# Optimization experiments

Measured on AMD Instinct MI355X. Metric: run time of the kernel, lower is better.

The kernel has to match this reference:

```python
import math
import jax, jax.numpy as jnp
import numpy as np

H = 12
D_MODEL = 768
D_K = D_MODEL // H
B, S = 2, 2048


def setup_inputs() -> dict:
    key = jax.random.key(0)
    ks = jax.random.split(key, 12)
    sc = 0.02
    inp = {
        "query": jax.random.normal(ks[0], (B, S, D_MODEL), jnp.float32),
        "key": jax.random.normal(ks[1], (B, S, D_MODEL), jnp.float32),
        "value": jax.random.normal(ks[2], (B, S, D_MODEL), jnp.float32),
        # causal mask [B, S, S]: 1 where attendable
        "mask": jnp.broadcast_to(jnp.tril(jnp.ones((S, S), jnp.int32)), (B, S, S)),
        "Wq": sc * jax.random.normal(ks[3], (D_MODEL, D_MODEL), jnp.float32),
        "bq": jnp.zeros((D_MODEL,), jnp.float32),
        "Wk": sc * jax.random.normal(ks[4], (D_MODEL, D_MODEL), jnp.float32),
        "bk": jnp.zeros((D_MODEL,), jnp.float32),
        "Wv": sc * jax.random.normal(ks[5], (D_MODEL, D_MODEL), jnp.float32),
        "bv": jnp.zeros((D_MODEL,), jnp.float32),
        "Wo": sc * jax.random.normal(ks[6], (D_MODEL, D_MODEL), jnp.float32),
        "bo": jnp.zeros((D_MODEL,), jnp.float32),
    }
    return inp


def reference(query, key, value, mask, Wq, bq, Wk, bk, Wv, bv, Wo, bo):
    b, s, _ = query.shape
    # linear projections (torch Linear: x @ W.T + b), split into heads
    def proj(x, W, bias):
        return (x @ W.T + bias).reshape(b, s, H, D_K).transpose(0, 2, 1, 3)  # [B,H,S,Dk]

    q = proj(query, Wq, bq)
    k = proj(key, Wk, bk)
    v = proj(value, Wv, bv)

    scores = jnp.einsum("bhqd,bhkd->bhqk", q, k) / math.sqrt(D_K)  # [B,H,S,S]
    # exponential time-decay bias over key positions 1..S, shape [1,1,1,S]
    time = jnp.exp(-jnp.arange(1, s + 1, dtype=scores.dtype))[None, None, None, :]
    scores = jnp.where(mask[:, None, :, :] == 0, jnp.asarray(-1e9, scores.dtype), scores)
    p_attn = jax.nn.softmax(scores - time, axis=-1)
    x = jnp.einsum("bhqk,bhkd->bhqd", p_attn, v)  # [B,H,S,Dk]
    x = x.transpose(0, 2, 1, 3).reshape(b, s, H * D_K)
    return x @ Wo.T + bo
```

## Files before the change

kernel.cpp:

```cpp
#include <hip/hip_runtime.h>
#include <hip/hip_bf16.h>
#include <math.h>

typedef __bf16 bf16;
typedef __attribute__((ext_vector_type(8))) __bf16 bf16x8;
typedef __attribute__((ext_vector_type(4))) __bf16 bf16x4;
typedef __attribute__((ext_vector_type(4))) float floatx4;

#define NH 12
#define DK 64
#define DM 768
#define NB 2
#define SEQ 2048
#define MTOT (NB * SEQ)
#define WELEM (DM * DM)
#define XELEM (MTOT * DM)

static __device__ __forceinline__ bf16x8 load8(const bf16* p) {
    return *(const bf16x8*)p;
}
static __device__ __forceinline__ float4 ld4(const float* p) {
    return *(const float4*)p;
}
static __device__ __forceinline__ bf16x8 cvt8(const float4 a, const float4 b) {
    bf16x8 r;
    r[0] = (bf16)a.x; r[1] = (bf16)a.y; r[2] = (bf16)a.z; r[3] = (bf16)a.w;
    r[4] = (bf16)b.x; r[5] = (bf16)b.y; r[6] = (bf16)b.z; r[7] = (bf16)b.w;
    return r;
}
static __device__ __forceinline__ void async16(const bf16* g, bf16* l) {
    __builtin_amdgcn_global_load_lds((const __attribute__((address_space(1))) void*)g,
                                     (__attribute__((address_space(3))) void*)l,
                                     16, 0, 0);
}

__global__ __launch_bounds__(256) void cvt_kernel(
    const float* __restrict__ wq, const float* __restrict__ wk,
    const float* __restrict__ wv, const float* __restrict__ wo,
    const float* __restrict__ xq, const float* __restrict__ xk, const float* __restrict__ xv,
    bf16* __restrict__ Wb, bf16* __restrict__ Wob,
    bf16* __restrict__ Xqb, bf16* __restrict__ Xkb, bf16* __restrict__ Xvb) {
    const int g = blockIdx.x * 256 + threadIdx.x;
    const int PW = WELEM / 8;
    const int PX = XELEM / 8;
    if (g < 4 * PW) {
        const int wi = g / PW;
        const int rem = g - wi * PW;
        const int n = rem / 96;
        const int t = rem - n * 96;
        const int s = t >> 3;
        const int j = t & 7;
        const float* src = (wi == 0) ? wq : (wi == 1) ? wk : (wi == 2) ? wv : wo;
        bf16* dst = (wi < 3) ? (Wb + (size_t)wi * WELEM) : Wob;
        const float* p = src + (size_t)n * DM + s * 64 + j * 8;
        *(bf16x8*)(dst + (size_t)n * DM + s * 64 + ((j ^ (n & 7)) * 8)) = cvt8(ld4(p), ld4(p + 4));
    } else {
        const int gx = g - 4 * PW;
        const int xi = gx / PX;
        const int rem = gx - xi * PX;
        const int m = rem / 96;
        const int t = rem - m * 96;
        const int s = t >> 3;
        const int j = t & 7;
        const float* src = (xi == 0) ? xq : (xi == 1) ? xk : xv;
        bf16* dst = (xi == 0) ? Xqb : (xi == 1) ? Xkb : Xvb;
        const float* p = src + (size_t)m * DM + s * 64 + j * 8;
        *(bf16x8*)(dst + (size_t)m * DM + s * 64 + ((j ^ (m & 7)) * 8)) = cvt8(ld4(p), ld4(p + 4));
    }
}

__global__ __launch_bounds__(256, 3) void qkv_kernel(
    const bf16* __restrict__ Xqb, const bf16* __restrict__ Xkb, const bf16* __restrict__ Xvb,
    const bf16* __restrict__ Wb,
    const float* __restrict__ bq, const float* __restrict__ bk, const float* __restrict__ bv,
    bf16* __restrict__ Oq, bf16* __restrict__ Ok, bf16* __restrict__ Ov) {
    __shared__ __align__(16) bf16 SM[2 * 64 * 64 + 2 * 128 * 64];
    bf16* As0 = SM;
    bf16* Bs0 = SM + 8192;

    const int tid = threadIdx.x;
    const int id = blockIdx.x;
    const int xcd = id & 7;
    const int sl = id >> 3;
    const int z = sl / 48;
    const int r = sl % 48;
    const int m0 = (xcd * 8 + r / 6) * 64;
    const int n0 = (r % 6) * 128;

    const bf16* X = (z == 0) ? Xqb : (z == 1) ? Xkb : Xvb;
    const bf16* W = Wb + (size_t)z * WELEM;
    const float* bias = (z == 0) ? bq : (z == 1) ? bk : bv;
    bf16* out = (z == 0) ? Oq : (z == 1) ? Ok : Ov;

    const int wv = tid >> 6;
    const int wm = wv >> 1, wn = wv & 1;
    const int lane = tid & 63;
    const int ln = lane & 15;
    const int kq = lane >> 4;
    const int drow = lane >> 3;
    const int dcol = (lane & 7) * 8;

    floatx4 acc[2][4];
#pragma unroll
    for (int i = 0; i < 2; i++)
#pragma unroll
        for (int j = 0; j < 4; j++) acc[i][j] = (floatx4){0.f, 0.f, 0.f, 0.f};

#pragma unroll
    for (int it = 0; it < 2; it++)
        async16(X + (size_t)(m0 + wv * 16 + it * 8 + drow) * DM + dcol,
                As0 + (wv * 16 + it * 8) * 64);
#pragma unroll
    for (int it = 0; it < 4; it++)
        async16(W + (size_t)(n0 + wv * 32 + it * 8 + drow) * DM + dcol,
                Bs0 + (wv * 32 + it * 8) * 64);

    for (int k = 0; k < 12; k++) {
        __syncthreads();
        const bf16* Ap = As0 + (k & 1) * 4096;
        const bf16* Bp = Bs0 + (k & 1) * 8192;
        if (k < 11) {
            const int kc = (k + 1) * 64;
            bf16* An = As0 + ((k + 1) & 1) * 4096;
            bf16* Bn = Bs0 + ((k + 1) & 1) * 8192;
#pragma unroll
            for (int it = 0; it < 2; it++)
                async16(X + (size_t)(m0 + wv * 16 + it * 8 + drow) * DM + kc + dcol,
                        An + (wv * 16 + it * 8) * 64);
#pragma unroll
            for (int it = 0; it < 4; it++)
                async16(W + (size_t)(n0 + wv * 32 + it * 8 + drow) * DM + kc + dcol,
                        Bn + (wv * 32 + it * 8) * 64);
        }
#pragma unroll
        for (int ks = 0; ks < 2; ks++) {
            const int jb = (ks * 4 + kq) ^ (ln & 7);
            bf16x8 af[2], bfm[4];
#pragma unroll
            for (int mt = 0; mt < 2; mt++)
                af[mt] = *(const bf16x8*)&Ap[(wm * 32 + mt * 16 + ln) * 64 + jb * 8];
#pragma unroll
            for (int nt = 0; nt < 4; nt++)
                bfm[nt] = *(const bf16x8*)&Bp[(wn * 64 + nt * 16 + ln) * 64 + jb * 8];
#pragma unroll
            for (int mt = 0; mt < 2; mt++)
#pragma unroll
                for (int nt = 0; nt < 4; nt++)
                    acc[mt][nt] = __builtin_amdgcn_mfma_f32_16x16x32_bf16(af[mt], bfm[nt], acc[mt][nt], 0, 0, 0);
        }
    }

    float bv4[4];
#pragma unroll
    for (int nt = 0; nt < 4; nt++) bv4[nt] = bias[n0 + wn * 64 + nt * 16 + ln];

    if (z < 2) {
        __syncthreads();
        bf16 (*E)[136] = (bf16(*)[136])SM;
#pragma unroll
        for (int mt = 0; mt < 2; mt++)
#pragma unroll
            for (int nt = 0; nt < 4; nt++)
#pragma unroll
                for (int r2 = 0; r2 < 4; r2++)
                    E[wm * 32 + mt * 16 + kq * 4 + r2][wn * 64 + nt * 16 + ln] =
                        (bf16)(acc[mt][nt][r2] + bv4[nt]);
        __syncthreads();
        const int row = tid >> 2;
        const int cb = (tid & 3) * 32;
        const int m = m0 + row;
        const int b = m >> 11;
        const int s = m & (SEQ - 1);
        const int h = (n0 + cb) >> 6;
        const int d = (n0 + cb) & 63;
        bf16* op = &out[((size_t)(b * NH + h) * SEQ + s) * DK + d];
#pragma unroll
        for (int q2 = 0; q2 < 4; q2++)
            *(bf16x8*)(op + q2 * 8) = *(bf16x8*)&E[row][cb + q2 * 8];
    } else {
        __syncthreads();
        bf16 (*E)[72] = (bf16(*)[72])SM;
#pragma unroll
        for (int nt = 0; nt < 4; nt++)
#pragma unroll
            for (int mt = 0; mt < 2; mt++) {
                bf16x4 v;
#pragma unroll
                for (int r2 = 0; r2 < 4; r2++) v[r2] = (bf16)(acc[mt][nt][r2] + bv4[nt]);
                *(bf16x4*)&E[wn * 64 + nt * 16 + ln][wm * 32 + mt * 16 + kq * 4] = v;
            }
        __syncthreads();
        const int row = tid >> 1;
        const int sc = (tid & 1) * 32;
        const int b = m0 >> 11;
        const int s0 = m0 & (SEQ - 1);
        const int h = (n0 >> 6) + (row >> 6);
        const int d = row & 63;
        bf16* op = &out[(size_t)(b * NH + h) * DK * SEQ + (size_t)d * SEQ + s0 + sc];
#pragma unroll
        for (int q2 = 0; q2 < 4; q2++)
            *(bf16x8*)(op + q2 * 8) = *(bf16x8*)&E[row][sc + q2 * 8];
    }
}

__global__ __launch_bounds__(256) void attn_kernel(const bf16* __restrict__ Q,
                                                   const bf16* __restrict__ K,
                                                   const bf16* __restrict__ Vt,
                                                   bf16* __restrict__ Xout) {
    __shared__ bf16 Ks[128][72];
    __shared__ bf16 Vs[64][136];
    __shared__ bf16 Ps[4][16][136];

    const int tid = threadIdx.x;
    const int wv = tid >> 6;
    const int lane = tid & 63;
    const int ln = lane & 15;
    const int kq = lane >> 4;
    const int krow = tid >> 1;
    const int kcol = (tid & 1) * 32;
    const int vrow = tid >> 2;
    const int vcol = (tid & 3) * 32;

    const int bidx = blockIdx.x;
    const int rk = (bidx < 256 || bidx >= 512) ? bidx : 767 - bidx;
    const int x = 31 - (rk / 24);
    const int bh = rk % 24;

    const int q0 = x * 64;
    const int qbase = q0 + wv * 16;
    const int nch = (x >> 1) + 1;

    const bf16* Qb = Q + (size_t)bh * SEQ * DK;
    const bf16* Kb = K + (size_t)bh * SEQ * DK;
    const bf16* Vb = Vt + (size_t)bh * SEQ * DK;

    const bf16x8 qa0 = load8(&Qb[(size_t)(qbase + ln) * DK + kq * 8]);
    const bf16x8 qa1 = load8(&Qb[(size_t)(qbase + ln) * DK + 32 + kq * 8]);

    bf16x8 kx[4], vx[4];
#pragma unroll
    for (int q = 0; q < 4; q++) {
        kx[q] = load8(&Kb[(size_t)krow * DK + kcol + q * 8]);
        vx[q] = load8(&Vb[(size_t)vrow * SEQ + vcol + q * 8]);
    }

    float lsum[4] = {0.f, 0.f, 0.f, 0.f};
    floatx4 Oacc[4];
#pragma unroll
    for (int nt = 0; nt < 4; nt++) Oacc[nt] = (floatx4){0.f, 0.f, 0.f, 0.f};

    int qg[4];
#pragma unroll
    for (int r = 0; r < 4; r++) qg[r] = qbase + kq * 4 + r;

    for (int c = 0; c < nch; c++) {
        const int k0 = c * 128;
        __syncthreads();
#pragma unroll
        for (int q = 0; q < 4; q++) {
            *(bf16x8*)&Ks[krow][kcol + q * 8] = kx[q];
            *(bf16x8*)&Vs[vrow][vcol + q * 8] = vx[q];
        }
        __syncthreads();
        if (c + 1 < nch) {
            const int kn = k0 + 128;
#pragma unroll
            for (int q = 0; q < 4; q++) {
                kx[q] = load8(&Kb[(size_t)(kn + krow) * DK + kcol + q * 8]);
                vx[q] = load8(&Vb[(size_t)vrow * SEQ + kn + vcol + q * 8]);
            }
        }

        floatx4 sc[8];
#pragma unroll
        for (int ks = 0; ks < 8; ks++) {
            const bf16x8 b0 = *(bf16x8*)&Ks[ks * 16 + ln][kq * 8];
            const bf16x8 b1 = *(bf16x8*)&Ks[ks * 16 + ln][32 + kq * 8];
            floatx4 t = (floatx4){0.f, 0.f, 0.f, 0.f};
            t = __builtin_amdgcn_mfma_f32_16x16x32_bf16(qa0, b0, t, 0, 0, 0);
            t = __builtin_amdgcn_mfma_f32_16x16x32_bf16(qa1, b1, t, 0, 0, 0);
            sc[ks] = t;
        }

        const bool last = (c == nch - 1);
#pragma unroll
        for (int ks = 0; ks < 8; ks++) {
            const int kg = k0 + ks * 16 + ln;
            const float tb = __expf(-(float)(kg + 1));
#pragma unroll
            for (int r = 0; r < 4; r++) {
                const float sv = sc[ks][r] * 0.125f - tb;
                float pf = __expf(sv);
                if (last && kg > qg[r]) pf = 0.f;
                const bf16 pb = (bf16)pf;
                Ps[wv][kq * 4 + r][ks * 16 + ln] = pb;
                lsum[r] += (float)pb;
            }
        }

        bf16x8 pa[4];
#pragma unroll
        for (int seg = 0; seg < 4; seg++) pa[seg] = *(bf16x8*)&Ps[wv][ln][seg * 32 + kq * 8];
#pragma unroll
        for (int nt = 0; nt < 4; nt++) {
#pragma unroll
            for (int seg = 0; seg < 4; seg++) {
                const bf16x8 vb = *(bf16x8*)&Vs[nt * 16 + ln][seg * 32 + kq * 8];
                Oacc[nt] = __builtin_amdgcn_mfma_f32_16x16x32_bf16(pa[seg], vb, Oacc[nt], 0, 0, 0);
            }
        }
    }

#pragma unroll
    for (int off = 1; off < 16; off <<= 1) {
#pragma unroll
        for (int r = 0; r < 4; r++) lsum[r] += __shfl_xor(lsum[r], off, 64);
    }
    float rl[4];
#pragma unroll
    for (int r = 0; r < 4; r++) rl[r] = 1.f / lsum[r];

    __syncthreads();
    bf16 (*E)[72] = (bf16(*)[72])Ks;
    const int erow = tid >> 2;
    const int ecb = (tid & 3) * 16;
#pragma unroll
    for (int nt = 0; nt < 4; nt++) {
#pragma unroll
        for (int r = 0; r < 4; r++)
            E[wv * 16 + kq * 4 + r][nt * 16 + ln] = (bf16)(Oacc[nt][r] * rl[r]);
    }
    __syncthreads();
    const int b = bh / NH;
    const int h = bh - b * NH;
    const int q = q0 + erow;
    const int j0 = (tid & 3) * 2;
    const int key = erow & 7;
    bf16* rowp = &Xout[((size_t)(b * SEQ + q)) * DM + h * DK];
    *(bf16x8*)(rowp + ((j0 ^ key) * 8)) = *(bf16x8*)&E[erow][ecb];
    *(bf16x8*)(rowp + (((j0 + 1) ^ key) * 8)) = *(bf16x8*)&E[erow][ecb + 8];
}

__global__ __launch_bounds__(256, 3) void outproj_kernel(const bf16* __restrict__ X,
                                                         const bf16* __restrict__ W,
                                                         const float* __restrict__ bias,
                                                         float* __restrict__ out) {
    __shared__ __align__(16) bf16 SM[2 * 64 * 64 + 2 * 128 * 64];
    bf16* As0 = SM;
    bf16* Bs0 = SM + 8192;

    const int tid = threadIdx.x;
    const int id = blockIdx.x;
    const int xcd = id & 7;
    const int sl = id >> 3;
    const int m0 = (xcd * 8 + sl / 6) * 64;
    const int n0 = (sl % 6) * 128;

    const int wv = tid >> 6;
    const int wm = wv >> 1, wn = wv & 1;
    const int lane = tid & 63;
    const int ln = lane & 15;
    const int kq = lane >> 4;
    const int drow = lane >> 3;
    const int dcol = (lane & 7) * 8;

    floatx4 acc[2][4];
#pragma unroll
    for (int i = 0; i < 2; i++)
#pragma unroll
        for (int j = 0; j < 4; j++) acc[i][j] = (floatx4){0.f, 0.f, 0.f, 0.f};

#pragma unroll
    for (int it = 0; it < 2; it++)
        async16(X + (size_t)(m0 + wv * 16 + it * 8 + drow) * DM + dcol,
                As0 + (wv * 16 + it * 8) * 64);
#pragma unroll
    for (int it = 0; it < 4; it++)
        async16(W + (size_t)(n0 + wv * 32 + it * 8 + drow) * DM + dcol,
                Bs0 + (wv * 32 + it * 8) * 64);

    for (int k = 0; k < 12; k++) {
        __syncthreads();
        const bf16* Ap = As0 + (k & 1) * 4096;
        const bf16* Bp = Bs0 + (k & 1) * 8192;
        if (k < 11) {
            const int kc = (k + 1) * 64;
            bf16* An = As0 + ((k + 1) & 1) * 4096;
            bf16* Bn = Bs0 + ((k + 1) & 1) * 8192;
#pragma unroll
            for (int it = 0; it < 2; it++)
                async16(X + (size_t)(m0 + wv * 16 + it * 8 + drow) * DM + kc + dcol,
                        An + (wv * 16 + it * 8) * 64);
#pragma unroll
            for (int it = 0; it < 4; it++)
                async16(W + (size_t)(n0 + wv * 32 + it * 8 + drow) * DM + kc + dcol,
                        Bn + (wv * 32 + it * 8) * 64);
        }
#pragma unroll
        for (int ks = 0; ks < 2; ks++) {
            const int jb = (ks * 4 + kq) ^ (ln & 7);
            bf16x8 af[2], bfm[4];
#pragma unroll
            for (int mt = 0; mt < 2; mt++)
                af[mt] = *(const bf16x8*)&Ap[(wm * 32 + mt * 16 + ln) * 64 + jb * 8];
#pragma unroll
            for (int nt = 0; nt < 4; nt++)
                bfm[nt] = *(const bf16x8*)&Bp[(wn * 64 + nt * 16 + ln) * 64 + jb * 8];
#pragma unroll
            for (int mt = 0; mt < 2; mt++)
#pragma unroll
                for (int nt = 0; nt < 4; nt++)
                    acc[mt][nt] = __builtin_amdgcn_mfma_f32_16x16x32_bf16(af[mt], bfm[nt], acc[mt][nt], 0, 0, 0);
        }
    }

#pragma unroll
    for (int nt = 0; nt < 4; nt++) {
        const int n = n0 + wn * 64 + nt * 16 + ln;
        const float bval = bias[n];
#pragma unroll
        for (int mt = 0; mt < 2; mt++)
#pragma unroll
            for (int r2 = 0; r2 < 4; r2++) {
                const int m = m0 + wm * 32 + mt * 16 + kq * 4 + r2;
                out[(size_t)m * DM + n] = acc[mt][nt][r2] + bval;
            }
    }
}

extern "C" void kernel_launch(void* const* d_in, const int* in_sizes, int n_in,
                              void* d_out, int out_size, void* d_ws, size_t ws_size,
                              hipStream_t stream) {
    const float* query = (const float*)d_in[0];
    const float* key   = (const float*)d_in[1];
    const float* value = (const float*)d_in[2];
    const float* Wq = (const float*)d_in[4];
    const float* bq = (const float*)d_in[5];
    const float* Wk = (const float*)d_in[6];
    const float* bk = (const float*)d_in[7];
    const float* Wv = (const float*)d_in[8];
    const float* bv = (const float*)d_in[9];
    const float* Wo = (const float*)d_in[10];
    const float* bo = (const float*)d_in[11];
    float* out = (float*)d_out;

    bf16* Qws  = (bf16*)d_ws;
    bf16* Kws  = Qws + XELEM;
    bf16* Vtws = Kws + XELEM;
    bf16* Xws  = Vtws + XELEM;
    bf16* Wob  = Xws + XELEM;
    bf16* Xvb  = Wob + WELEM;

    bf16* Wb  = (bf16*)out;
    bf16* Xkb = (bf16*)out + 3 * WELEM;

    bf16* Xqb = Xws;

    const int ncvt = (4 * (WELEM / 8) + 3 * (XELEM / 8)) / 256;
    cvt_kernel<<<ncvt, 256, 0, stream>>>(Wq, Wk, Wv, Wo, query, key, value,
                                         Wb, Wob, Xqb, Xkb, Xvb);

    qkv_kernel<<<1152, 256, 0, stream>>>(Xqb, Xkb, Xvb, Wb, bq, bk, bv,
                                         Qws, Kws, Vtws);

    attn_kernel<<<768, 256, 0, stream>>>(Qws, Kws, Vtws, Xws);

    outproj_kernel<<<384, 256, 0, stream>>>(Xws, Wob, bo, out);
}
```

Before: 195.0 us.

## Double-buffer K/V tiles via async LDS loads with swizzled layout

The attention kernel now streams K and V in 64-key chunks into double-buffered LDS using global_load_lds async copies instead of staging through registers. The projection epilogue pre-swizzles K and Vt rows with an XOR pattern so LDS reads are bank-conflict free without padding. Q is pre-scaled by log2(e)/sqrt(dk) so softmax uses exp2f directly, and the time-decay bias is only computed on the first chunk because it is negligible later. Smaller chunks mean finer causal skipping but twice as many loop iterations and barriers. The bias truncation relies on exp(-k) underflowing in float.

After: 204.1 us. +4.7%, slower.

```diff
diff --git a/kernel.cpp b/kernel.cpp
--- a/kernel.cpp
+++ b/kernel.cpp
@@ -15,6 +15,7 @@
 #define MTOT (NB * SEQ)
 #define WELEM (DM * DM)
 #define XELEM (MTOT * DM)
+#define QSCALE 0.18033688f
 
 static __device__ __forceinline__ bf16x8 load8(const bf16* p) {
     return *(const bf16x8*)p;
@@ -153,6 +154,7 @@
     float bv4[4];
 #pragma unroll
     for (int nt = 0; nt < 4; nt++) bv4[nt] = bias[n0 + wn * 64 + nt * 16 + ln];
+    const float sc = (z == 0) ? QSCALE : 1.0f;
 
     if (z < 2) {
         __syncthreads();
@@ -164,7 +166,7 @@
 #pragma unroll
                 for (int r2 = 0; r2 < 4; r2++)
                     E[wm * 32 + mt * 16 + kq * 4 + r2][wn * 64 + nt * 16 + ln] =
-                        (bf16)(acc[mt][nt][r2] + bv4[nt]);
+                        (bf16)((acc[mt][nt][r2] + bv4[nt]) * sc);
         __syncthreads();
         const int row = tid >> 2;
         const int cb = (tid & 3) * 32;
@@ -172,11 +174,12 @@
         const int b = m >> 11;
         const int s = m & (SEQ - 1);
         const int h = (n0 + cb) >> 6;
-        const int d = (n0 + cb) & 63;
-        bf16* op = &out[((size_t)(b * NH + h) * SEQ + s) * DK + d];
+        const int key = (z == 1) ? (row & 7) : 0;
+        bf16* op = &out[((size_t)(b * NH + h) * SEQ + s) * DK];
+        const int jbase = (cb & 63) >> 3;
 #pragma unroll
         for (int q2 = 0; q2 < 4; q2++)
-            *(bf16x8*)(op + q2 * 8) = *(bf16x8*)&E[row][cb + q2 * 8];
+            *(bf16x8*)(op + ((jbase + q2) ^ key) * 8) = *(bf16x8*)&E[row][cb + q2 * 8];
     } else {
         __syncthreads();
         bf16 (*E)[72] = (bf16(*)[72])SM;
@@ -191,15 +194,17 @@
             }
         __syncthreads();
         const int row = tid >> 1;
-        const int sc = (tid & 1) * 32;
+        const int scc = (tid & 1) * 32;
         const int b = m0 >> 11;
         const int s0 = m0 & (SEQ - 1);
         const int h = (n0 >> 6) + (row >> 6);
         const int d = row & 63;
-        bf16* op = &out[(size_t)(b * NH + h) * DK * SEQ + (size_t)d * SEQ + s0 + sc];
+        const int key = d & 7;
+        bf16* op = &out[(size_t)(b * NH + h) * DK * SEQ + (size_t)d * SEQ + s0];
+        const int jbase = scc >> 3;
 #pragma unroll
         for (int q2 = 0; q2 < 4; q2++)
-            *(bf16x8*)(op + q2 * 8) = *(bf16x8*)&E[row][sc + q2 * 8];
+            *(bf16x8*)(op + ((jbase + q2) ^ key) * 8) = *(bf16x8*)&E[row][scc + q2 * 8];
     }
 }
 
@@ -207,19 +212,17 @@
                                                    const bf16* __restrict__ K,
                                                    const bf16* __restrict__ Vt,
                                                    bf16* __restrict__ Xout) {
-    __shared__ bf16 Ks[128][72];
-    __shared__ bf16 Vs[64][136];
-    __shared__ bf16 Ps[4][16][136];
+    __shared__ __align__(16) bf16 Ks[2][64 * 64];
+    __shared__ __align__(16) bf16 Vs[2][64 * 64];
+    __shared__ bf16 Ps[4][16][68];
 
     const int tid = threadIdx.x;
     const int wv = tid >> 6;
     const int lane = tid & 63;
     const int ln = lane & 15;
     const int kq = lane >> 4;
-    const int krow = tid >> 1;
-    const int kcol = (tid & 1) * 32;
-    const int vrow = tid >> 2;
-    const int vcol = (tid & 3) * 32;
+    const int drow = lane >> 3;
+    const int dcol = (lane & 7) * 8;
 
     const int bidx = blockIdx.x;
     const int rk = (bidx < 256 || bidx >= 512) ? bidx : 767 - bidx;
@@ -228,21 +231,25 @@
 
     const int q0 = x * 64;
     const int qbase = q0 + wv * 16;
-    const int nch = (x >> 1) + 1;
+    const int nch = x + 1;
 
     const bf16* Qb = Q + (size_t)bh * SEQ * DK;
     const bf16* Kb = K + (size_t)bh * SEQ * DK;
     const bf16* Vb = Vt + (size_t)bh * SEQ * DK;
 
+#pragma unroll
+    for (int it = 0; it < 2; it++) {
+        async16(Kb + (size_t)(wv * 16 + it * 8 + drow) * DK + dcol,
+                &Ks[0][(wv * 16 + it * 8) * 64]);
+        async16(Vb + (size_t)(wv * 16 + it * 8 + drow) * SEQ + dcol,
+                &Vs[0][(wv * 16 + it * 8) * 64]);
+    }
+
     const bf16x8 qa0 = load8(&Qb[(size_t)(qbase + ln) * DK + kq * 8]);
     const bf16x8 qa1 = load8(&Qb[(size_t)(qbase + ln) * DK + 32 + kq * 8]);
 
-    bf16x8 kx[4], vx[4];
-#pragma unroll
-    for (int q = 0; q < 4; q++) {
-        kx[q] = load8(&Kb[(size_t)krow * DK + kcol + q * 8]);
-        vx[q] = load8(&Vb[(size_t)vrow * SEQ + vcol + q * 8]);
-    }
+    const int e0 = (kq ^ (ln & 7)) * 8;
+    const int e1 = ((kq + 4) ^ (ln & 7)) * 8;
 
     float lsum[4] = {0.f, 0.f, 0.f, 0.f};
     floatx4 Oacc[4];
@@ -254,60 +261,55 @@
     for (int r = 0; r < 4; r++) qg[r] = qbase + kq * 4 + r;
 
     for (int c = 0; c < nch; c++) {
-        const int k0 = c * 128;
-        __syncthreads();
-#pragma unroll
-        for (int q = 0; q < 4; q++) {
-            *(bf16x8*)&Ks[krow][kcol + q * 8] = kx[q];
-            *(bf16x8*)&Vs[vrow][vcol + q * 8] = vx[q];
-        }
+        const int k0 = c * 64;
+        const int buf = c & 1;
         __syncthreads();
         if (c + 1 < nch) {
-            const int kn = k0 + 128;
-#pragma unroll
-            for (int q = 0; q < 4; q++) {
-                kx[q] = load8(&Kb[(size_t)(kn + krow) * DK + kcol + q * 8]);
-                vx[q] = load8(&Vb[(size_t)vrow * SEQ + kn + vcol + q * 8]);
+            const int kn = k0 + 64;
+            const int nb = buf ^ 1;
+#pragma unroll
+            for (int it = 0; it < 2; it++) {
+                async16(Kb + (size_t)(kn + wv * 16 + it * 8 + drow) * DK + dcol,
+                        &Ks[nb][(wv * 16 + it * 8) * 64]);
+                async16(Vb + (size_t)(wv * 16 + it * 8 + drow) * SEQ + kn + dcol,
+                        &Vs[nb][(wv * 16 + it * 8) * 64]);
             }
         }
 
-        floatx4 sc[8];
-#pragma unroll
-        for (int ks = 0; ks < 8; ks++) {
-            const bf16x8 b0 = *(bf16x8*)&Ks[ks * 16 + ln][kq * 8];
-            const bf16x8 b1 = *(bf16x8*)&Ks[ks * 16 + ln][32 + kq * 8];
+        floatx4 sc[4];
+#pragma unroll
+        for (int ks = 0; ks < 4; ks++) {
+            const bf16x8 b0 = *(const bf16x8*)&Ks[buf][(ks * 16 + ln) * 64 + e0];
+            const bf16x8 b1 = *(const bf16x8*)&Ks[buf][(ks * 16 + ln) * 64 + e1];
             floatx4 t = (floatx4){0.f, 0.f, 0.f, 0.f};
             t = __builtin_amdgcn_mfma_f32_16x16x32_bf16(qa0, b0, t, 0, 0, 0);
             t = __builtin_amdgcn_mfma_f32_16x16x32_bf16(qa1, b1, t, 0, 0, 0);
             sc[ks] = t;
         }
 
-        const bool last = (c == nch - 1);
-#pragma unroll
-        for (int ks = 0; ks < 8; ks++) {
+        const bool last = (c == x);
+#pragma unroll
+        for (int ks = 0; ks < 4; ks++) {
             const int kg = k0 + ks * 16 + ln;
-            const float tb = __expf(-(float)(kg + 1));
+            float tb2 = 0.f;
+            if (c == 0) tb2 = 1.44269504f * __expf(-(float)(kg + 1));
 #pragma unroll
             for (int r = 0; r < 4; r++) {
-                const float sv = sc[ks][r] * 0.125f - tb;
-                float pf = __expf(sv);
+                float pf = exp2f(sc[ks][r] - tb2);
                 if (last && kg > qg[r]) pf = 0.f;
-                const bf16 pb = (bf16)pf;
-                Ps[wv][kq * 4 + r][ks * 16 + ln] = pb;
-                lsum[r] += (float)pb;
+                Ps[wv][kq * 4 + r][ks * 16 + ln] = (bf16)pf;
+                lsum[r] += pf;
             }
         }
 
-        bf16x8 pa[4];
-#pragma unroll
-        for (int seg = 0; seg < 4; seg++) pa[seg] = *(bf16x8*)&Ps[wv][ln][seg * 32 + kq * 8];
+        const bf16x8 pa0 = *(const bf16x8*)&Ps[wv][ln][kq * 8];
+        const bf16x8 pa1 = *(const bf16x8*)&Ps[wv][ln][32 + kq * 8];
 #pragma unroll
         for (int nt = 0; nt < 4; nt++) {
-#pragma unroll
-            for (int seg = 0; seg < 4; seg++) {
-                const bf16x8 vb = *(bf16x8*)&Vs[nt * 16 + ln][seg * 32 + kq * 8];
-                Oacc[nt] = __builtin_amdgcn_mfma_f32_16x16x32_bf16(pa[seg], vb, Oacc[nt], 0, 0, 0);
-            }
+            const bf16x8 v0 = *(const bf16x8*)&Vs[buf][(nt * 16 + ln) * 64 + e0];
+            const bf16x8 v1 = *(const bf16x8*)&Vs[buf][(nt * 16 + ln) * 64 + e1];
+            Oacc[nt] = __builtin_amdgcn_mfma_f32_16x16x32_bf16(pa0, v0, Oacc[nt], 0, 0, 0);
+            Oacc[nt] = __builtin_amdgcn_mfma_f32_16x16x32_bf16(pa1, v1, Oacc[nt], 0, 0, 0);
         }
     }
 
```
